# Performance work log

Measured on AMD Instinct MI355X. Metric: run time of the kernel, lower is better.

The kernel has to match this reference:

```python
import jax, jax.numpy as jnp
import numpy as np

EPS = 1e-5  # torch LayerNorm default


def _ln(v, g, b):
    m = jnp.mean(v, axis=-1, keepdims=True)
    var = jnp.var(v, axis=-1, keepdims=True)
    return (v - m) / jnp.sqrt(var + EPS) * g + b


def setup_inputs() -> dict:
    key = jax.random.key(0)
    ks = jax.random.split(key, 12)
    S, E, H = 4096, 1024, 8
    s = 0.02  # weight scale ~ nn.Linear init magnitude
    return {
        "x": jax.random.normal(ks[0], (S, E), jnp.float32),
        "Wq": jax.random.normal(ks[1], (H, E, E), jnp.float32) * s,
        "bq": jax.random.normal(ks[2], (H, E), jnp.float32) * s,
        "Wk": jax.random.normal(ks[3], (H, E, E), jnp.float32) * s,
        "bk": jax.random.normal(ks[4], (H, E), jnp.float32) * s,
        "Wv": jax.random.normal(ks[5], (H, E, E), jnp.float32) * s,
        "bv": jax.random.normal(ks[6], (H, E), jnp.float32) * s,
        "Wz": jax.random.normal(ks[7], (E, H * E), jnp.float32) * s,
        "bz": jax.random.normal(ks[8], (E,), jnp.float32) * s,
        "g1": jnp.ones((E,), jnp.float32),
        "b1": jnp.zeros((E,), jnp.float32),
        "Wf": jax.random.normal(ks[9], (E, E), jnp.float32) * s,
        "bf": jax.random.normal(ks[10], (E,), jnp.float32) * s,
        "g2": jnp.ones((E,), jnp.float32),
        "b2": jnp.zeros((E,), jnp.float32),
    }


def reference(x, Wq, bq, Wk, bk, Wv, bv, Wz, bz, g1, b1, Wf, bf, g2, b2):
    S, E = x.shape
    # per-head projections, batched over heads: y_h = x @ W_h.T + b_h
    Q = jnp.einsum('se,hoe->hso', x, Wq) + bq[:, None, :]  # [H,S,E]
    K = jnp.einsum('se,hoe->hso', x, Wk) + bk[:, None, :]
    V = jnp.einsum('se,hoe->hso', x, Wv) + bv[:, None, :]
    # non-standard attention: scores = K^T @ Q over the sequence dim -> [H,E,E]
    scores = jnp.einsum('hse,hsf->hef', K, Q) / jnp.sqrt(jnp.float32(E))
    A = jax.nn.softmax(scores, axis=-1)  # torch softmax(dim=1) on [E,E]
    Zh = jnp.einsum('hse,hef->hsf', V, A)  # [H,S,E]
    # concat heads along feature dim -> [S, H*E]
    Z = jnp.transpose(Zh, (1, 0, 2)).reshape(S, -1)
    O = Z @ Wz.T + bz
    LN1 = _ln(O, g1, b1) + x
    FN = LN1 @ Wf.T + bf
    LN2 = _ln(FN, g2, b2) + LN1
    return LN2
```

## Files before the change

kernel.cpp:

```cpp
#include <hip/hip_runtime.h>

#define S_DIM 4096
#define E_DIM 1024
#define H_DIM 8

typedef __bf16 bf16x8 __attribute__((ext_vector_type(8)));
typedef float  f32x4  __attribute__((ext_vector_type(4)));

__device__ __forceinline__ void async16(const __bf16* gsrc, __bf16* lbase, int lane)
{
#if __has_builtin(__builtin_amdgcn_global_load_lds)
    __builtin_amdgcn_global_load_lds(
        (const __attribute__((address_space(1))) unsigned int*)gsrc,
        (__attribute__((address_space(3))) unsigned int*)lbase, 16, 0, 0);
#else
    ((int4*)lbase)[lane] = *(const int4*)gsrc;
#endif
}

template <int MODE>
__device__ __forceinline__ void stage_op(const __bf16* __restrict__ src, int ld,
                                         int mn0, int k0, __bf16* lds, int tid)
{
    if constexpr (MODE == 0) {
        const int w = tid >> 6, l = tid & 63;
        const int r8 = l >> 3, c8 = (l & 7) << 3;
#pragma unroll
        for (int i = 0; i < 4; i++) {
            const int rbase = w * 32 + i * 8;
            const __bf16* g = src + (size_t)(mn0 + rbase + r8) * ld + k0 + c8;
            async16(g, &lds[rbase * 64], l);
        }
    } else {
        const int cg = tid & 15, kg = tid >> 4;
        __bf16 h[4][8];
#pragma unroll
        for (int r = 0; r < 4; r++) {
            const __bf16* s = src + (size_t)(k0 + kg * 4 + r) * ld + mn0 + cg * 8;
            *(int4*)&h[r][0] = *(const int4*)s;
        }
        const int xr = cg & 7;
#pragma unroll
        for (int j = 0; j < 8; j++) {
            union { __bf16 q[4]; unsigned long long v; } u;
            u.q[0]=h[0][j]; u.q[1]=h[1][j]; u.q[2]=h[2][j]; u.q[3]=h[3][j];
            const int scol = cg * 8 + (j ^ xr);
            *(unsigned long long*)&lds[scol * 72 + kg * 4] = u.v;
        }
    }
}

template <int AM, int BM, int OUT>
__global__ __launch_bounds__(256) void gemm128(
    const __bf16* __restrict__ Ag, const __bf16* __restrict__ Bg,
    void* __restrict__ Cg, const float* __restrict__ biasg,
    int Klen, int kPerZ, int lda, int ldb, int ldc,
    long long sA, long long sB, long long sC, float scale)
{
    __shared__ __bf16 As[128 * 72];
    __shared__ __bf16 Bs[128 * 72];
    constexpr int SA = (AM == 2) ? 72 : 64;
    constexpr int SB = (BM == 2) ? 72 : 64;

    const int tid  = threadIdx.x;
    const int lane = tid & 63;
    const int wave = tid >> 6;
    const int t    = lane & 15;
    const int quad = lane >> 4;
    const int wm   = wave >> 1;
    const int wn   = wave & 1;
    const int m0   = blockIdx.y * 128;
    const int n0   = blockIdx.x * 128;
    const size_t zi = blockIdx.z;

    const __bf16* A = (kPerZ == 0) ? Ag + zi * sA : Ag;
    const __bf16* B = (kPerZ == 0) ? Bg + zi * sB : Bg;
    const int kbeg = kPerZ ? (int)zi * kPerZ : 0;

    int rowA[4], rowB[4];
#pragma unroll
    for (int i = 0; i < 4; i++) {
        int ra = wm * 64 + i * 16 + t;
        int rb = wn * 64 + i * 16 + t;
        rowA[i] = (AM == 2) ? (ra ^ ((ra >> 3) & 7)) : ra;
        rowB[i] = (BM == 2) ? (rb ^ ((rb >> 3) & 7)) : rb;
    }

    f32x4 acc[4][4];
#pragma unroll
    for (int i = 0; i < 4; i++)
#pragma unroll
        for (int j = 0; j < 4; j++) { f32x4 z = {0.f,0.f,0.f,0.f}; acc[i][j] = z; }

    for (int k0 = kbeg; k0 < kbeg + Klen; k0 += 64) {
        stage_op<AM>(A, lda, m0, k0, As, tid);
        stage_op<BM>(B, ldb, n0, k0, Bs, tid);
        __syncthreads();
#pragma unroll
        for (int kk = 0; kk < 2; kk++) {
            bf16x8 af[4], bfv[4];
#pragma unroll
            for (int i = 0; i < 4; i++)
                af[i] = *(const bf16x8*)(&As[rowA[i] * SA + kk*32 + quad*8]);
#pragma unroll
            for (int j = 0; j < 4; j++)
                bfv[j] = *(const bf16x8*)(&Bs[rowB[j] * SB + kk*32 + quad*8]);
#pragma unroll
            for (int i = 0; i < 4; i++)
#pragma unroll
                for (int j = 0; j < 4; j++)
                    acc[i][j] = __builtin_amdgcn_mfma_f32_16x16x32_bf16(af[i], bfv[j], acc[i][j], 0, 0, 0);
        }
        __syncthreads();
    }

#pragma unroll
    for (int i = 0; i < 4; i++) {
        const int rowb = m0 + wm*64 + i*16 + quad*4;
#pragma unroll
        for (int j = 0; j < 4; j++) {
            const int col = n0 + wn*64 + j*16 + t;
            const float bv = biasg ? biasg[col] : 0.f;
#pragma unroll
            for (int r = 0; r < 4; r++) {
                const float v = acc[i][j][r] * scale + bv;
                if constexpr (OUT == 0) {
                    __bf16* C = (__bf16*)Cg + zi * sC;
                    C[(size_t)(rowb + r) * ldc + col] = (__bf16)v;
                } else if constexpr (OUT == 1) {
                    float* C = (float*)Cg + zi * sC;
                    C[(size_t)(rowb + r) * ldc + col] = v;
                } else {
                    float* C = (float*)Cg;
                    atomicAdd(&C[(size_t)(rowb + r) * ldc + col], v);
                }
            }
        }
    }
}

template <int OUT>
__global__ __launch_bounds__(512, 1) void gemmP(
    const __bf16* __restrict__ Ag, const __bf16* __restrict__ Bg,
    void* __restrict__ Cg, int Klen, int kPerZ,
    int lda, int ldb, int ldc, long long sBhead, long long sC,
    int nMt, int mtpx)
{
    __shared__ __bf16 sm[2 * 24576];

    const int tid  = threadIdx.x;
    const int lane = tid & 63;
    const int wave = tid >> 6;
    const int wm = wave >> 1, wn = wave & 1;
    const int t = lane & 15, q = lane >> 4;

    const int bid = blockIdx.x;
    const int bpz = nMt << 3;
    const int zi  = bid / bpz;
    const int rr  = bid - zi * bpz;
    int mt, nt;
    if (mtpx > 0) {
        const int xcd = rr & 7, s = rr >> 3;
        mt = xcd * mtpx + (s >> 3);
        nt = s & 7;
    } else {
        mt = rr >> 3;
        nt = rr & 7;
    }
    const int m0 = mt * 256;
    const int n0 = nt * 128;
    const int kbeg = zi * kPerZ;
    const int NT = Klen >> 6;

    const __bf16* Bp = Bg + (size_t)(m0 >> 10) * sBhead;

    const int gslot = ((lane & 7) ^ (lane >> 3)) & 7;
    const int lrow  = lane >> 3;

    auto stage_sub = [&](int kt, int which) {
        __bf16* base = &sm[(kt & 1) * 24576 + which * 8192 + wave * 512];
        const int k0 = kbeg + kt * 64;
#pragma unroll
        for (int p = 0; p < 2; p++) {
            const int idx = p * 64 + wave * 8 + lrow;
            int grow;
            const __bf16* src;
            int ld;
            if (which == 2) { grow = n0 + idx; src = Bp; ld = ldb; }
            else {
                grow = m0 + (((idx >> 5) << 6) | (idx & 31)) + (which ? 32 : 0);
                src = Ag; ld = lda;
            }
            async16(src + (size_t)grow * ld + k0 + gslot * 8, base + p * 4096, lane);
        }
    };

    const int fx = t & 7;

    f32x4 acc[4][4];
#pragma unroll
    for (int i = 0; i < 4; i++)
#pragma unroll
        for (int j = 0; j < 4; j++) { f32x4 z = {0.f,0.f,0.f,0.f}; acc[i][j] = z; }

    stage_sub(0, 0); stage_sub(0, 2); stage_sub(0, 1);

    for (int kt = 0; kt < NT; ++kt) {
        const __bf16* ba = &sm[(kt & 1) * 24576];
        const __bf16* bb = ba + 8192;
        const __bf16* bB = ba + 16384;

        if (kt + 1 < NT) {
            stage_sub(kt + 1, 0); stage_sub(kt + 1, 2);
            asm volatile("s_waitcnt vmcnt(6)" ::: "memory");
        } else {
            asm volatile("s_waitcnt vmcnt(2)" ::: "memory");
        }
        __builtin_amdgcn_s_barrier();
        __builtin_amdgcn_sched_barrier(0);

        bf16x8 bfr[4][2], afr[2][2];
#pragma unroll
        for (int j = 0; j < 4; j++)
#pragma unroll
            for (int kk = 0; kk < 2; kk++)
                bfr[j][kk] = *(const bf16x8*)&bB[(wn*64 + j*16 + t) * 64 + (((kk<<2)|q) ^ fx) * 8];
#pragma unroll
        for (int i = 0; i < 2; i++)
#pragma unroll
            for (int kk = 0; kk < 2; kk++)
                afr[i][kk] = *(const bf16x8*)&ba[(wm*32 + i*16 + t) * 64 + (((kk<<2)|q) ^ fx) * 8];

        __builtin_amdgcn_s_setprio(1);
#pragma unroll
        for (int i = 0; i < 2; i++)
#pragma unroll
            for (int kk = 0; kk < 2; kk++)
#pragma unroll
                for (int j = 0; j < 4; j++)
                    acc[i][j] = __builtin_amdgcn_mfma_f32_16x16x32_bf16(afr[i][kk], bfr[j][kk], acc[i][j], 0, 0, 0);
        __builtin_amdgcn_s_setprio(0);
        __builtin_amdgcn_s_barrier();
        __builtin_amdgcn_sched_barrier(0);

        if (kt + 1 < NT) {
            stage_sub(kt + 1, 1);
            asm volatile("s_waitcnt vmcnt(6)" ::: "memory");
        } else {
            asm volatile("s_waitcnt vmcnt(0)" ::: "memory");
        }
        __builtin_amdgcn_s_barrier();
        __builtin_amdgcn_sched_barrier(0);

        bf16x8 afr2[2][2];
#pragma unroll
        for (int i = 0; i < 2; i++)
#pragma unroll
            for (int kk = 0; kk < 2; kk++)
                afr2[i][kk] = *(const bf16x8*)&bb[(wm*32 + i*16 + t) * 64 + (((kk<<2)|q) ^ fx) * 8];

        __builtin_amdgcn_s_setprio(1);
#pragma unroll
        for (int i = 0; i < 2; i++)
#pragma unroll
            for (int kk = 0; kk < 2; kk++)
#pragma unroll
                for (int j = 0; j < 4; j++)
                    acc[i+2][j] = __builtin_amdgcn_mfma_f32_16x16x32_bf16(afr2[i][kk], bfr[j][kk], acc[i+2][j], 0, 0, 0);
        __builtin_amdgcn_s_setprio(0);
        __builtin_amdgcn_s_barrier();
        __builtin_amdgcn_sched_barrier(0);
    }

#pragma unroll
    for (int i = 0; i < 4; i++) {
        const int rowb = m0 + wm * 64 + i * 16 + q * 4;
#pragma unroll
        for (int j = 0; j < 4; j++) {
            const int col = n0 + wn * 64 + j * 16 + t;
#pragma unroll
            for (int r = 0; r < 4; r++) {
                const float v = acc[i][j][r];
                if constexpr (OUT == 0) {
                    ((__bf16*)Cg)[(size_t)(rowb + r) * ldc + col] = (__bf16)v;
                } else {
                    float* C = (float*)Cg + (size_t)zi * sC;
                    C[(size_t)(rowb + r) * ldc + col] = v;
                }
            }
        }
    }
}

__global__ __launch_bounds__(256) void cvt_bf16(
    const float* __restrict__ in, __bf16* __restrict__ out)
{
    const size_t i = ((size_t)blockIdx.x * 256 + threadIdx.x) * 8;
    float4 a = *(const float4*)(in + i);
    float4 b = *(const float4*)(in + i + 4);
    union { __bf16 h[8]; int4 v; } u;
    u.h[0]=(__bf16)a.x; u.h[1]=(__bf16)a.y; u.h[2]=(__bf16)a.z; u.h[3]=(__bf16)a.w;
    u.h[4]=(__bf16)b.x; u.h[5]=(__bf16)b.y; u.h[6]=(__bf16)b.z; u.h[7]=(__bf16)b.w;
    *(int4*)(out + i) = u.v;
}

__global__ __launch_bounds__(256) void sum8_cvt(
    const float* __restrict__ P, __bf16* __restrict__ out)
{
    const size_t EE = (size_t)E_DIM * E_DIM;
    const size_t i = ((size_t)blockIdx.x * 256 + threadIdx.x) * 8;
    float4 a = {0.f,0.f,0.f,0.f}, b = {0.f,0.f,0.f,0.f};
#pragma unroll
    for (int p = 0; p < 8; p++) {
        float4 x = *(const float4*)(P + p*EE + i);
        float4 y = *(const float4*)(P + p*EE + i + 4);
        a.x+=x.x; a.y+=x.y; a.z+=x.z; a.w+=x.w;
        b.x+=y.x; b.y+=y.y; b.z+=y.z; b.w+=y.w;
    }
    union { __bf16 h[8]; int4 v; } u;
    u.h[0]=(__bf16)a.x; u.h[1]=(__bf16)a.y; u.h[2]=(__bf16)a.z; u.h[3]=(__bf16)a.w;
    u.h[4]=(__bf16)b.x; u.h[5]=(__bf16)b.y; u.h[6]=(__bf16)b.z; u.h[7]=(__bf16)b.w;
    *(int4*)(out + i) = u.v;
}

__global__ __launch_bounds__(256) void colsum_u(const float* __restrict__ x, float* __restrict__ u)
{
    const int c = threadIdx.x * 4;
    float4 a = {0.f,0.f,0.f,0.f};
    const int r0 = blockIdx.x * 64;
    for (int r = 0; r < 64; r++) {
        float4 v = *(const float4*)(x + (size_t)(r0 + r) * E_DIM + c);
        a.x += v.x; a.y += v.y; a.z += v.z; a.w += v.w;
    }
    atomicAdd(&u[c+0], a.x); atomicAdd(&u[c+1], a.y);
    atomicAdd(&u[c+2], a.z); atomicAdd(&u[c+3], a.w);
}

__global__ __launch_bounds__(256) void gemv_u(
    const float* __restrict__ Wk, const float* __restrict__ Wq,
    const float* __restrict__ u, float* __restrict__ kq, float* __restrict__ qq)
{
    const int gw = blockIdx.x * 4 + (threadIdx.x >> 6);
    const int lane = threadIdx.x & 63;
    const float* W = (gw < 8192) ? Wk + (size_t)gw * E_DIM
                                 : Wq + (size_t)(gw - 8192) * E_DIM;
    float s = 0.f;
#pragma unroll
    for (int i = 0; i < 4; i++) {
        float4 w = *(const float4*)(W + lane*16 + i*4);
        float4 z = *(const float4*)(u + lane*16 + i*4);
        s += w.x*z.x + w.y*z.y + w.z*z.z + w.w*z.w;
    }
#pragma unroll
    for (int o = 32; o > 0; o >>= 1) s += __shfl_down(s, o);
    if (lane == 0) { if (gw < 8192) kq[gw] = s; else qq[gw - 8192] = s; }
}

__global__ __launch_bounds__(256) void colsum_zb(
    const __bf16* __restrict__ Ab, const float* __restrict__ bv, float* __restrict__ zb)
{
    const int h = blockIdx.y;
    const int f = blockIdx.x * 256 + threadIdx.x;
    const int o0 = blockIdx.z * 256;
    const __bf16* A = Ab + (size_t)h * E_DIM * E_DIM + (size_t)o0 * E_DIM + f;
    const float* bvh = bv + h * E_DIM + o0;
    float s = 0.f;
    for (int o = 0; o < 256; o++) s += bvh[o] * (float)A[(size_t)o * E_DIM];
    atomicAdd(&zb[h * E_DIM + f], s);
}

__global__ __launch_bounds__(256) void gemv_oc(
    const float* __restrict__ Wz, const float* __restrict__ zb,
    const float* __restrict__ bz, float* __restrict__ oc)
{
    const int gw = blockIdx.x * 4 + (threadIdx.x >> 6);
    const int lane = threadIdx.x & 63;
    const float* W = Wz + (size_t)gw * (H_DIM * E_DIM);
    float s = 0.f;
#pragma unroll
    for (int i = 0; i < 32; i++) {
        float4 w = *(const float4*)(W + i*256 + lane*4);
        float4 z = *(const float4*)(zb + i*256 + lane*4);
        s += w.x*z.x + w.y*z.y + w.z*z.z + w.w*z.w;
    }
#pragma unroll
    for (int o = 32; o > 0; o >>= 1) s += __shfl_down(s, o);
    if (lane == 0) oc[gw] = s + bz[gw];
}

__global__ __launch_bounds__(256) void softmax_fused(
    const float* __restrict__ Sc, const float* __restrict__ kq,
    const float* __restrict__ qq, const float* __restrict__ bk,
    const float* __restrict__ bq, __bf16* __restrict__ Aout)
{
    __shared__ float red[4];
    const int row = blockIdx.x;
    const int h = row >> 10;
    const int tid = threadIdx.x, lane = tid & 63, wave = tid >> 6;
    const float kqj = kq[row], bkj = bk[row];
    const float cst = (float)S_DIM * bkj;

    float4 v = ((const float4*)(Sc + (size_t)row * E_DIM))[tid];
    const int c = tid * 4;
    float4 qv = *(const float4*)(qq + (h << 10) + c);
    float4 bv = *(const float4*)(bq + (h << 10) + c);
    v.x = (v.x + kqj*bv.x + bkj*qv.x + cst*bv.x) * 0.03125f;
    v.y = (v.y + kqj*bv.y + bkj*qv.y + cst*bv.y) * 0.03125f;
    v.z = (v.z + kqj*bv.z + bkj*qv.z + cst*bv.z) * 0.03125f;
    v.w = (v.w + kqj*bv.w + bkj*qv.w + cst*bv.w) * 0.03125f;

    float m = fmaxf(fmaxf(v.x, v.y), fmaxf(v.z, v.w));
#pragma unroll
    for (int o = 32; o > 0; o >>= 1) m = fmaxf(m, __shfl_down(m, o));
    if (lane == 0) red[wave] = m;
    __syncthreads();
    m = fmaxf(fmaxf(red[0], red[1]), fmaxf(red[2], red[3]));
    __syncthreads();

    const float e0 = __expf(v.x - m), e1 = __expf(v.y - m);
    const float e2 = __expf(v.z - m), e3 = __expf(v.w - m);
    float s = e0 + e1 + e2 + e3;
#pragma unroll
    for (int o = 32; o > 0; o >>= 1) s += __shfl_down(s, o);
    if (lane == 0) red[wave] = s;
    __syncthreads();
    s = red[0] + red[1] + red[2] + red[3];
    const float inv = 1.f / s;

    __bf16* out = Aout + (size_t)row * E_DIM + c;
    out[0] = (__bf16)(e0*inv); out[1] = (__bf16)(e1*inv);
    out[2] = (__bf16)(e2*inv); out[3] = (__bf16)(e3*inv);
}

template <int NPART, bool CB, bool WRITE_BF16>
__global__ __launch_bounds__(256) void ln_residual(
    const float* __restrict__ X, const float* __restrict__ cb,
    const float* __restrict__ resid,
    const float* __restrict__ g, const float* __restrict__ b,
    __bf16* __restrict__ outB, float* __restrict__ outF)
{
    __shared__ float redS[4], redQ[4];
    const int row = blockIdx.x;
    const int tid = threadIdx.x, lane = tid & 63, wave = tid >> 6;
    const size_t SE = (size_t)S_DIM * E_DIM;

    float4 v = ((const float4*)(X + (size_t)row * E_DIM))[tid];
#pragma unroll
    for (int p = 1; p < NPART; ++p) {
        float4 v1 = ((const float4*)(X + (size_t)p * SE + (size_t)row * E_DIM))[tid];
        v.x += v1.x; v.y += v1.y; v.z += v1.z; v.w += v1.w;
    }
    if constexpr (CB) {
        float4 cv = ((const float4*)cb)[tid];
        v.x += cv.x; v.y += cv.y; v.z += cv.z; v.w += cv.w;
    }
    float s = v.x + v.y + v.z + v.w;
    float q = v.x*v.x + v.y*v.y + v.z*v.z + v.w*v.w;
#pragma unroll
    for (int o = 32; o > 0; o >>= 1) { s += __shfl_down(s, o); q += __shfl_down(q, o); }
    if (lane == 0) { redS[wave] = s; redQ[wave] = q; }
    __syncthreads();
    s = redS[0]+redS[1]+redS[2]+redS[3];
    q = redQ[0]+redQ[1]+redQ[2]+redQ[3];

    const float mean = s * (1.f / E_DIM);
    const float var  = q * (1.f / E_DIM) - mean * mean;
    const float rstd = rsqrtf(var + 1e-5f);

    const int c0 = tid * 4;
    float4 rv = ((const float4*)(resid + (size_t)row * E_DIM))[tid];
    const float res[4] = {rv.x, rv.y, rv.z, rv.w};
    const float* vp = &v.x;
#pragma unroll
    for (int i = 0; i < 4; i++) {
        const float o = (vp[i] - mean) * rstd * g[c0+i] + b[c0+i] + res[i];
        outF[(size_t)row * E_DIM + c0 + i] = o;
        if constexpr (WRITE_BF16) outB[(size_t)row * E_DIM + c0 + i] = (__bf16)o;
    }
}

extern "C" void kernel_launch(void* const* d_in, const int* in_sizes, int n_in,
                              void* d_out, int out_size, void* d_ws, size_t ws_size,
                              hipStream_t stream)
{
    const float* x   = (const float*)d_in[0];
    const float* Wq  = (const float*)d_in[1];
    const float* bq  = (const float*)d_in[2];
    const float* Wk  = (const float*)d_in[3];
    const float* bk  = (const float*)d_in[4];
    const float* Wv  = (const float*)d_in[5];
    const float* bv  = (const float*)d_in[6];
    const float* Wz  = (const float*)d_in[7];
    const float* bz  = (const float*)d_in[8];
    const float* g1  = (const float*)d_in[9];
    const float* b1  = (const float*)d_in[10];
    const float* Wf  = (const float*)d_in[11];
    const float* bfp = (const float*)d_in[12];
    const float* g2  = (const float*)d_in[13];
    const float* b2  = (const float*)d_in[14];

    char* ws = (char*)d_ws;
    const long long EE = (long long)E_DIM * E_DIM;
    const long long SE = (long long)S_DIM * E_DIM;
    const size_t MB = 1024ull * 1024ull;

    __bf16* xb   = (__bf16*)(ws);
    __bf16* Wqb  = (__bf16*)(ws +   8*MB);
    __bf16* Wkb  = (__bf16*)(ws +  24*MB);
    __bf16* Wvb  = (__bf16*)(ws +  40*MB);
    __bf16* Wzb  = (__bf16*)(ws +  56*MB);
    __bf16* Wfb  = (__bf16*)(ws +  72*MB);
    float*  Gf   = (float*) (ws +  74*MB);
    __bf16* Gb   = (__bf16*)(ws +  78*MB);
    __bf16* PTb  = (__bf16*)(ws +  84*MB);
    float*  u    = (float*) (ws +  86*MB);
    float*  kq   = (float*) (ws +  86*MB +  65536);
    float*  qq   = (float*) (ws +  86*MB + 131072);
    float*  zb   = (float*) (ws +  86*MB + 196608);
    float*  oc   = (float*) (ws +  86*MB + 262144);
    __bf16* LN1b = (__bf16*)(ws +  87*MB);
    float*  LN1f = (float*) (ws +  95*MB);
    __bf16* Tb   = (__bf16*)(ws + 111*MB);
    float*  Sc   = (float*) (ws + 127*MB);
    __bf16* Ab   = (__bf16*)(ws + 159*MB);
    __bf16* Mcat = (__bf16*)(ws + 175*MB);
    float*  PTp  = (float*) (ws + 111*MB);
    float*  Ob   = (float*) (ws + 111*MB);
    float*  FNb  = (float*) (ws + 111*MB);

    dim3 blk(256);
    dim3 blk5(512);

    hipMemsetAsync(Gf,  0, 4*MB, stream);
    hipMemsetAsync(u,   0, E_DIM*4, stream);
    hipMemsetAsync(zb,  0, H_DIM*E_DIM*4, stream);

    cvt_bf16<<<dim3(2048), blk, 0, stream>>>(x,  xb);
    cvt_bf16<<<dim3(4096), blk, 0, stream>>>(Wq, Wqb);
    cvt_bf16<<<dim3(4096), blk, 0, stream>>>(Wk, Wkb);
    cvt_bf16<<<dim3(4096), blk, 0, stream>>>(Wv, Wvb);
    cvt_bf16<<<dim3(4096), blk, 0, stream>>>(Wz, Wzb);
    cvt_bf16<<<dim3(512),  blk, 0, stream>>>(Wf, Wfb);

    colsum_u<<<dim3(64), blk, 0, stream>>>(x, u);
    gemv_u<<<dim3(4096), blk, 0, stream>>>(Wk, Wq, u, kq, qq);

    gemm128<2, 2, 2><<<dim3(8, 8, 8), blk, 0, stream>>>(
        xb, xb, (void*)Gf, nullptr, 512, 512, E_DIM, E_DIM, E_DIM, 0, 0, 0, 1.f);
    cvt_bf16<<<dim3(512), blk, 0, stream>>>(Gf, Gb);

    gemmP<0><<<dim3(256), blk5, 0, stream>>>(
        Wkb, Gb, (void*)Tb, 1024, 0, E_DIM, E_DIM, E_DIM, 0, 0, 32, 4);
    gemmP<1><<<dim3(256), blk5, 0, stream>>>(
        Tb, Wqb, (void*)Sc, 1024, 0, E_DIM, E_DIM, E_DIM, EE, 0, 32, 4);
    softmax_fused<<<dim3(H_DIM * E_DIM), blk, 0, stream>>>(Sc, kq, qq, bk, bq, Ab);

    gemm128<2, 2, 0><<<dim3(8, 8, 8), blk, 0, stream>>>(
        Wvb, Ab, (void*)Mcat, nullptr, E_DIM, 0, E_DIM, E_DIM, H_DIM * E_DIM,
        EE, EE, E_DIM, 1.f);
    colsum_zb<<<dim3(4, 8, 4), blk, 0, stream>>>(Ab, bv, zb);
    gemv_oc<<<dim3(256), blk, 0, stream>>>(Wz, zb, bz, oc);

    gemmP<1><<<dim3(256), blk5, 0, stream>>>(
        Wzb, Mcat, (void*)PTp, 1024, 1024, H_DIM * E_DIM, H_DIM * E_DIM,
        E_DIM, 0, EE, 4, 0);
    sum8_cvt<<<dim3(512), blk, 0, stream>>>(PTp, PTb);

    gemmP<1><<<dim3(256), blk5, 0, stream>>>(
        xb, PTb, (void*)Ob, 512, 512, E_DIM, E_DIM, E_DIM, 0, SE, 16, 2);
    ln_residual<2, true, true><<<dim3(S_DIM), blk, 0, stream>>>(
        Ob, oc, x, g1, b1, LN1b, LN1f);

    gemmP<1><<<dim3(256), blk5, 0, stream>>>(
        LN1b, Wfb, (void*)FNb, 512, 512, E_DIM, E_DIM, E_DIM, 0, SE, 16, 2);
    ln_residual<2, true, false><<<dim3(S_DIM), blk, 0, stream>>>(
        FNb, bfp, LN1f, g2, b2, nullptr, (float*)d_out);
}
```

Baseline: 478.6 us.

## Reassociate V-path products and route all GEMMs through pipelined gemmP kernel

Removes the simple gemm128 kernel and makes gemmP generic over A/B addressing modes (per-head and split-K strides). The Gram matrix x^T x is now computed from a transposed bf16 copy of x with split-K into partial buffers and a sum8 reduction, replacing the atomicAdd path and its memset. The V path is reassociated: Wz_h·A_h^T is computed first, then multiplied by transposed Wv, which needs a new transpose-convert kernel for Wv and x. The intent is to use the double-buffered 256x128 kernel everywhere and drop atomics, at the cost of an extra transpose pass and more partial-sum traffic.

```diff
diff --git a/kernel.cpp b/kernel.cpp
--- a/kernel.cpp
+++ b/kernel.cpp
@@ -18,132 +18,11 @@
 #endif
 }
 
-template <int MODE>
-__device__ __forceinline__ void stage_op(const __bf16* __restrict__ src, int ld,
-                                         int mn0, int k0, __bf16* lds, int tid)
-{
-    if constexpr (MODE == 0) {
-        const int w = tid >> 6, l = tid & 63;
-        const int r8 = l >> 3, c8 = (l & 7) << 3;
-#pragma unroll
-        for (int i = 0; i < 4; i++) {
-            const int rbase = w * 32 + i * 8;
-            const __bf16* g = src + (size_t)(mn0 + rbase + r8) * ld + k0 + c8;
-            async16(g, &lds[rbase * 64], l);
-        }
-    } else {
-        const int cg = tid & 15, kg = tid >> 4;
-        __bf16 h[4][8];
-#pragma unroll
-        for (int r = 0; r < 4; r++) {
-            const __bf16* s = src + (size_t)(k0 + kg * 4 + r) * ld + mn0 + cg * 8;
-            *(int4*)&h[r][0] = *(const int4*)s;
-        }
-        const int xr = cg & 7;
-#pragma unroll
-        for (int j = 0; j < 8; j++) {
-            union { __bf16 q[4]; unsigned long long v; } u;
-            u.q[0]=h[0][j]; u.q[1]=h[1][j]; u.q[2]=h[2][j]; u.q[3]=h[3][j];
-            const int scol = cg * 8 + (j ^ xr);
-            *(unsigned long long*)&lds[scol * 72 + kg * 4] = u.v;
-        }
-    }
-}
-
-template <int AM, int BM, int OUT>
-__global__ __launch_bounds__(256) void gemm128(
-    const __bf16* __restrict__ Ag, const __bf16* __restrict__ Bg,
-    void* __restrict__ Cg, const float* __restrict__ biasg,
-    int Klen, int kPerZ, int lda, int ldb, int ldc,
-    long long sA, long long sB, long long sC, float scale)
-{
-    __shared__ __bf16 As[128 * 72];
-    __shared__ __bf16 Bs[128 * 72];
-    constexpr int SA = (AM == 2) ? 72 : 64;
-    constexpr int SB = (BM == 2) ? 72 : 64;
-
-    const int tid  = threadIdx.x;
-    const int lane = tid & 63;
-    const int wave = tid >> 6;
-    const int t    = lane & 15;
-    const int quad = lane >> 4;
-    const int wm   = wave >> 1;
-    const int wn   = wave & 1;
-    const int m0   = blockIdx.y * 128;
-    const int n0   = blockIdx.x * 128;
-    const size_t zi = blockIdx.z;
-
-    const __bf16* A = (kPerZ == 0) ? Ag + zi * sA : Ag;
-    const __bf16* B = (kPerZ == 0) ? Bg + zi * sB : Bg;
-    const int kbeg = kPerZ ? (int)zi * kPerZ : 0;
-
-    int rowA[4], rowB[4];
-#pragma unroll
-    for (int i = 0; i < 4; i++) {
-        int ra = wm * 64 + i * 16 + t;
-        int rb = wn * 64 + i * 16 + t;
-        rowA[i] = (AM == 2) ? (ra ^ ((ra >> 3) & 7)) : ra;
-        rowB[i] = (BM == 2) ? (rb ^ ((rb >> 3) & 7)) : rb;
-    }
-
-    f32x4 acc[4][4];
-#pragma unroll
-    for (int i = 0; i < 4; i++)
-#pragma unroll
-        for (int j = 0; j < 4; j++) { f32x4 z = {0.f,0.f,0.f,0.f}; acc[i][j] = z; }
-
-    for (int k0 = kbeg; k0 < kbeg + Klen; k0 += 64) {
-        stage_op<AM>(A, lda, m0, k0, As, tid);
-        stage_op<BM>(B, ldb, n0, k0, Bs, tid);
-        __syncthreads();
-#pragma unroll
-        for (int kk = 0; kk < 2; kk++) {
-            bf16x8 af[4], bfv[4];
-#pragma unroll
-            for (int i = 0; i < 4; i++)
-                af[i] = *(const bf16x8*)(&As[rowA[i] * SA + kk*32 + quad*8]);
-#pragma unroll
-            for (int j = 0; j < 4; j++)
-                bfv[j] = *(const bf16x8*)(&Bs[rowB[j] * SB + kk*32 + quad*8]);
-#pragma unroll
-            for (int i = 0; i < 4; i++)
-#pragma unroll
-                for (int j = 0; j < 4; j++)
-                    acc[i][j] = __builtin_amdgcn_mfma_f32_16x16x32_bf16(af[i], bfv[j], acc[i][j], 0, 0, 0);
-        }
-        __syncthreads();
-    }
-
-#pragma unroll
-    for (int i = 0; i < 4; i++) {
-        const int rowb = m0 + wm*64 + i*16 + quad*4;
-#pragma unroll
-        for (int j = 0; j < 4; j++) {
-            const int col = n0 + wn*64 + j*16 + t;
-            const float bv = biasg ? biasg[col] : 0.f;
-#pragma unroll
-            for (int r = 0; r < 4; r++) {
-                const float v = acc[i][j][r] * scale + bv;
-                if constexpr (OUT == 0) {
-                    __bf16* C = (__bf16*)Cg + zi * sC;
-                    C[(size_t)(rowb + r) * ldc + col] = (__bf16)v;
-                } else if constexpr (OUT == 1) {
-                    float* C = (float*)Cg + zi * sC;
-                    C[(size_t)(rowb + r) * ldc + col] = v;
-                } else {
-                    float* C = (float*)Cg;
-                    atomicAdd(&C[(size_t)(rowb + r) * ldc + col], v);
-                }
-            }
-        }
-    }
-}
-
-template <int OUT>
+template <int OUT, int AM, int BM>
 __global__ __launch_bounds__(512, 1) void gemmP(
     const __bf16* __restrict__ Ag, const __bf16* __restrict__ Bg,
     void* __restrict__ Cg, int Klen, int kPerZ,
-    int lda, int ldb, int ldc, long long sBhead, long long sC,
+    int lda, int ldb, int ldc, long long sA, long long sB, long long sC,
     int nMt, int mtpx)
 {
     __shared__ __bf16 sm[2 * 24576];
@@ -172,26 +51,34 @@
     const int kbeg = zi * kPerZ;
     const int NT = Klen >> 6;
 
-    const __bf16* Bp = Bg + (size_t)(m0 >> 10) * sBhead;
-
     const int gslot = ((lane & 7) ^ (lane >> 3)) & 7;
     const int lrow  = lane >> 3;
 
     auto stage_sub = [&](int kt, int which) {
         __bf16* base = &sm[(kt & 1) * 24576 + which * 8192 + wave * 512];
-        const int k0 = kbeg + kt * 64;
+        const int kk = kbeg + kt * 64;
 #pragma unroll
         for (int p = 0; p < 2; p++) {
             const int idx = p * 64 + wave * 8 + lrow;
-            int grow;
-            const __bf16* src;
-            int ld;
-            if (which == 2) { grow = n0 + idx; src = Bp; ld = ldb; }
-            else {
-                grow = m0 + (((idx >> 5) << 6) | (idx & 31)) + (which ? 32 : 0);
-                src = Ag; ld = lda;
+            const __bf16* g;
+            if (which == 2) {
+                const int grow = n0 + idx;
+                if constexpr (BM == 1)
+                    g = Bg + (size_t)(m0 >> 10) * sB + (size_t)grow * ldb + kk + gslot * 8;
+                else if constexpr (BM == 2)
+                    g = Bg + (size_t)(kk >> 10) * sB + (size_t)grow * ldb + (kk & 1023) + gslot * 8;
+                else
+                    g = Bg + (size_t)grow * ldb + kk + gslot * 8;
+            } else {
+                const int grow = m0 + (((idx >> 5) << 6) | (idx & 31)) + (which ? 32 : 0);
+                if constexpr (AM == 1)
+                    g = Ag + (size_t)(m0 >> 10) * sA + (size_t)(grow & 1023) * lda + kk + gslot * 8;
+                else if constexpr (AM == 2)
+                    g = Ag + (size_t)(kk >> 10) * sA + (size_t)grow * lda + (kk & 1023) + gslot * 8;
+                else
+                    g = Ag + (size_t)grow * lda + kk + gslot * 8;
             }
-            async16(src + (size_t)grow * ld + k0 + gslot * 8, base + p * 4096, lane);
+            async16(g, base + p * 4096, lane);
         }
     };
 
@@ -289,6 +176,39 @@
                 }
             }
         }
+    }
+}
+
+template <bool WN>
+__global__ __launch_bounds__(256) void trans_cvt(
+    const float* __restrict__ in, __bf16* __restrict__ outT,
+    __bf16* __restrict__ outN, int R, int C)
+{
+    __shared__ float t[64][65];
+    const size_t base = (size_t)blockIdx.z * R * C;
+    const int r0 = blockIdx.y * 64, c0 = blockIdx.x * 64;
+    const int tid = threadIdx.x;
+    const int r = tid >> 2;
+#pragma unroll
+    for (int i = 0; i < 4; i++) {
+        const int j = (tid & 3) + i * 4;
+        float4 v = *(const float4*)(in + base + (size_t)(r0 + r) * C + c0 + j * 4);
+        t[r][j*4+0] = v.x; t[r][j*4+1] = v.y; t[r][j*4+2] = v.z; t[r][j*4+3] = v.w;
+        if constexpr (WN) {
+            union { __bf16 h[4]; unsigned long long q; } u;
+            u.h[0]=(__bf16)v.x; u.h[1]=(__bf16)v.y; u.h[2]=(__bf16)v.z; u.h[3]=(__bf16)v.w;
+            *(unsigned long long*)(outN + base + (size_t)(r0 + r) * C + c0 + j * 4) = u.q;
+        }
+    }
+    __syncthreads();
+#pragma unroll
+    for (int i = 0; i < 2; i++) {
+        const int idx = tid + 256 * i;
+        const int c = idx >> 3, h8 = idx & 7;
+        union { __bf16 h[8]; int4 q; } u;
+#pragma unroll
+        for (int k = 0; k < 8; k++) u.h[k] = (__bf16)t[h8*8+k][c];
+        *(int4*)(outT + base + (size_t)(c0 + c) * R + r0 + h8 * 8) = u.q;
     }
 }
 
@@ -507,12 +427,12 @@
     __bf16* xb   = (__bf16*)(ws);
     __bf16* Wqb  = (__bf16*)(ws +   8*MB);
     __bf16* Wkb  = (__bf16*)(ws +  24*MB);
-    __bf16* Wvb  = (__bf16*)(ws +  40*MB);
+    __bf16* WvT  = (__bf16*)(ws +  40*MB);
     __bf16* Wzb  = (__bf16*)(ws +  56*MB);
     __bf16* Wfb  = (__bf16*)(ws +  72*MB);
-    float*  Gf   = (float*) (ws +  74*MB);
-    __bf16* Gb   = (__bf16*)(ws +  78*MB);
-    __bf16* PTb  = (__bf16*)(ws +  84*MB);
+    __bf16* Gb   = (__bf16*)(ws +  74*MB);
+    __bf16* PTb  = (__bf16*)(ws +  76*MB);
+    __bf16* xbT  = (__bf16*)(ws +  78*MB);
     float*  u    = (float*) (ws +  86*MB);
     float*  kq   = (float*) (ws +  86*MB +  65536);
     float*  qq   = (float*) (ws +  86*MB + 131072);
@@ -523,7 +443,8 @@
     __bf16* Tb   = (__bf16*)(ws + 111*MB);
     float*  Sc   = (float*) (ws + 127*MB);
     __bf16* Ab   = (__bf16*)(ws + 159*MB);
-    __bf16* Mcat = (__bf16*)(ws + 175*MB);
+    __bf16* Yb   = (__bf16*)(ws + 175*MB);
+    float*  Gp   = (float*) (ws + 111*MB);
     float*  PTp  = (float*) (ws + 111*MB);
     float*  Ob   = (float*) (ws + 111*MB);
     float*  FNb  = (float*) (ws + 111*MB);
@@ -531,48 +452,46 @@
     dim3 blk(256);
     dim3 blk5(512);
 
-    hipMemsetAsync(Gf,  0, 4*MB, stream);
     hipMemsetAsync(u,   0, E_DIM*4, stream);
     hipMemsetAsync(zb,  0, H_DIM*E_DIM*4, stream);
 
-    cvt_bf16<<<dim3(2048), blk, 0, stream>>>(x,  xb);
+    trans_cvt<true><<<dim3(16, 64, 1), blk, 0, stream>>>(x, xbT, xb, S_DIM, E_DIM);
     cvt_bf16<<<dim3(4096), blk, 0, stream>>>(Wq, Wqb);
     cvt_bf16<<<dim3(4096), blk, 0, stream>>>(Wk, Wkb);
-    cvt_bf16<<<dim3(4096), blk, 0, stream>>>(Wv, Wvb);
     cvt_bf16<<<dim3(4096), blk, 0, stream>>>(Wz, Wzb);
     cvt_bf16<<<dim3(512),  blk, 0, stream>>>(Wf, Wfb);
+    trans_cvt<false><<<dim3(16, 16, 8), blk, 0, stream>>>(Wv, WvT, nullptr, E_DIM, E_DIM);
 
     colsum_u<<<dim3(64), blk, 0, stream>>>(x, u);
     gemv_u<<<dim3(4096), blk, 0, stream>>>(Wk, Wq, u, kq, qq);
 
-    gemm128<2, 2, 2><<<dim3(8, 8, 8), blk, 0, stream>>>(
-        xb, xb, (void*)Gf, nullptr, 512, 512, E_DIM, E_DIM, E_DIM, 0, 0, 0, 1.f);
-    cvt_bf16<<<dim3(512), blk, 0, stream>>>(Gf, Gb);
-
-    gemmP<0><<<dim3(256), blk5, 0, stream>>>(
-        Wkb, Gb, (void*)Tb, 1024, 0, E_DIM, E_DIM, E_DIM, 0, 0, 32, 4);
-    gemmP<1><<<dim3(256), blk5, 0, stream>>>(
-        Tb, Wqb, (void*)Sc, 1024, 0, E_DIM, E_DIM, E_DIM, EE, 0, 32, 4);
+    gemmP<1, 0, 0><<<dim3(256), blk5, 0, stream>>>(
+        xbT, xbT, (void*)Gp, 512, 512, S_DIM, S_DIM, E_DIM, 0, 0, EE, 4, 0);
+    sum8_cvt<<<dim3(512), blk, 0, stream>>>(Gp, Gb);
+
+    gemmP<0, 0, 0><<<dim3(256), blk5, 0, stream>>>(
+        Wkb, Gb, (void*)Tb, 1024, 0, E_DIM, E_DIM, E_DIM, 0, 0, 0, 32, 4);
+    gemmP<1, 0, 1><<<dim3(256), blk5, 0, stream>>>(
+        Tb, Wqb, (void*)Sc, 1024, 0, E_DIM, E_DIM, E_DIM, 0, EE, 0, 32, 4);
     softmax_fused<<<dim3(H_DIM * E_DIM), blk, 0, stream>>>(Sc, kq, qq, bk, bq, Ab);
 
-    gemm128<2, 2, 0><<<dim3(8, 8, 8), blk, 0, stream>>>(
-        Wvb, Ab, (void*)Mcat, nullptr, E_DIM, 0, E_DIM, E_DIM, H_DIM * E_DIM,
-        EE, EE, E_DIM, 1.f);
+    gemmP<0, 1, 1><<<dim3(256), blk5, 0, stream>>>(
+        Wzb, Ab, (void*)Yb, 1024, 0, H_DIM * E_DIM, E_DIM, E_DIM, E_DIM, EE, 0, 32, 4);
+
     colsum_zb<<<dim3(4, 8, 4), blk, 0, stream>>>(Ab, bv, zb);
     gemv_oc<<<dim3(256), blk, 0, stream>>>(Wz, zb, bz, oc);
 
-    gemmP<1><<<dim3(256), blk5, 0, stream>>>(
-        Wzb, Mcat, (void*)PTp, 1024, 1024, H_DIM * E_DIM, H_DIM * E_DIM,
-        E_DIM, 0, EE, 4, 0);
+    gemmP<1, 2, 2><<<dim3(256), blk5, 0, stream>>>(
+        Yb, WvT, (void*)PTp, 1024, 1024, E_DIM, E_DIM, E_DIM, EE, EE, EE, 4, 0);
     sum8_cvt<<<dim3(512), blk, 0, stream>>>(PTp, PTb);
 
-    gemmP<1><<<dim3(256), blk5, 0, stream>>>(
-        xb, PTb, (void*)Ob, 512, 512, E_DIM, E_DIM, E_DIM, 0, SE, 16, 2);
+    gemmP<1, 0, 0><<<dim3(256), blk5, 0, stream>>>(
+        xb, PTb, (void*)Ob, 512, 512, E_DIM, E_DIM, E_DIM, 0, 0, SE, 16, 2);
     ln_residual<2, true, true><<<dim3(S_DIM), blk, 0, stream>>>(
         Ob, oc, x, g1, b1, LN1b, LN1f);
 
-    gemmP<1><<<dim3(256), blk5, 0, stream>>>(
-        LN1b, Wfb, (void*)FNb, 512, 512, E_DIM, E_DIM, E_DIM, 0, SE, 16, 2);
+    gemmP<1, 0, 0><<<dim3(256), blk5, 0, stream>>>(
+        LN1b, Wfb, (void*)FNb, 512, 512, E_DIM, E_DIM, E_DIM, 0, 0, SE, 16, 2);
     ln_residual<2, true, false><<<dim3(S_DIM), blk, 0, stream>>>(
         FNb, bfp, LN1f, g2, b2, nullptr, (float*)d_out);
 }
```

Measured after the change: 453.6 us. 5.2% less time.
